# Kernel tuning notes

Measured on AMD Instinct MI355X. Metric: run time of the kernel, lower is better.

Reference implementation:

```python
import jax, jax.numpy as jnp
import numpy as np

N_POINTS = 262144
NUM_ENC = 6      # F
NUM_FEATS = 16   # C
LOG2_RES = 5
STD = 0.2


def setup_inputs() -> dict:
    key = jax.random.key(0)
    k1, k2 = jax.random.split(key)
    points = jax.random.normal(k1, (N_POINTS, 3), dtype=jnp.float32)
    # freqs = 2 ** linspace(0, F-1, F) = [1,2,4,8,16,32]
    freqs = 2.0 ** jnp.linspace(0.0, NUM_ENC - 1.0, NUM_ENC).astype(jnp.float32)
    res = 2 ** LOG2_RES
    features = jax.random.normal(k2, (NUM_ENC * 2 * 3, NUM_FEATS, res, 1), dtype=jnp.float32) * STD
    return {"points": points, "freqs": freqs, "features": features}


def _forward(points, freqs, features):
    n = points.shape[0]
    F = freqs.shape[0]
    C = features.shape[1]
    res = features.shape[2]
    # --- pos_encode ---
    fp = points[:, None, :] * freqs[None, :, None]          # (n, F, 3)
    enc = jnp.stack((jnp.sin(fp), jnp.cos(fp)), axis=-2)    # (n, F, 2, 3)
    encs = enc.reshape(n, F * 2 * 3).T                       # (G=F*2*3, n), values in [-1,1]
    # --- encoder: grid_sample(features, grid=[x=0, y=encs], align_corners=True) ---
    # features: (G, C, H=res, W=1); x=0 with W=1 -> column 0; bilinear only along H.
    g = jnp.transpose(features[..., 0], (0, 2, 1))           # (G, res, C)
    iy = (encs + 1.0) * 0.5 * (res - 1)                      # (G, n), align_corners=True mapping
    iy0 = jnp.floor(iy)
    w1 = iy - iy0                                            # weight for upper neighbor
    i0 = jnp.clip(iy0.astype(jnp.int32), 0, res - 1)
    i1 = jnp.clip(i0 + 1, 0, res - 1)                        # clamp safe: w1==0 at boundary
    take = jax.vmap(lambda tbl, idx: tbl[idx])               # per-grid gather
    v0 = take(g, i0)                                         # (G, n, C)
    v1 = take(g, i1)                                         # (G, n, C)
    fs = v0 * (1.0 - w1)[..., None] + v1 * w1[..., None]     # (G, n, C)
    fs = jnp.swapaxes(fs, 1, 2)                              # (G, C, n), matches torch (G,C,1,N)
    # raw contiguous reinterpretation (36 -> F,3,2) exactly as torch .view does
    fs = fs.reshape(F, 3, 2, C, n) + encs.reshape(F, 3, 2, 1, n)
    return jnp.transpose(fs, (4, 3, 0, 1, 2)).reshape(n, -1)  # (n, C*F*3*2)


def reference(points, freqs, features):
    return _forward(points, freqs, features)
```

## Files before the change

kernel.cpp:

```cpp
#include <hip/hip_runtime.h>

#define NPTS   262144
#define CHUNK  256
#define BLOCK  1024
#define NG     36
#define NC     16
#define RES    32
#define TAB_FLOATS (NG * NC * RES)


__global__ __launch_bounds__(BLOCK) void freqhash_kernel(
    const float* __restrict__ points,
    const float* __restrict__ features,
    float* __restrict__ out)
{
    __shared__ float tab[TAB_FLOATS + 4];
    __shared__ float sval[CHUNK * NG];

    const int t = threadIdx.x;
    const int chunk_base = blockIdx.x * CHUNK;

    {
        const float4* __restrict__ src = (const float4*)features;
        float4* dst = (float4*)tab;
        #pragma unroll
        for (int i = 0; i < TAB_FLOATS / 4 / BLOCK + 1; ++i) {
            int idx = t + i * BLOCK;
            if (idx < TAB_FLOATS / 4) dst[idx] = src[idx];
        }
        if (t == 0) {
            tab[TAB_FLOATS + 0] = 0.f; tab[TAB_FLOATS + 1] = 0.f;
            tab[TAB_FLOATS + 2] = 0.f; tab[TAB_FLOATS + 3] = 0.f;
        }
    }

    {
        const int phat    = t >> 2;
        const int quarter = t & 3;
        const int p = chunk_base + phat;
        const float x = points[p * 3 + 0];
        const float y = points[p * 3 + 1];
        const float z = points[p * 3 + 2];
        #pragma unroll
        for (int k = 0; k < 9; ++k) {
            const int g   = quarter * 9 + k;
            const int f   = g / 6;
            const int rem = g - f * 6;
            const int s   = rem / 3;
            const int d   = rem - s * 3;
            const float coord = (d == 0) ? x : ((d == 1) ? y : z);
            const float freq  = (float)(1 << f);
            const float rev   = coord * freq * 0.15915494309189535f;
            const float r     = __builtin_amdgcn_fractf(rev);
            const float sv    = __builtin_amdgcn_sinf(r);
            const float cv    = __builtin_amdgcn_cosf(r);
            const float val   = s ? cv : sv;
            sval[t * 9 + k] = val;
        }
    }
    __syncthreads();

    float* __restrict__ outp = out + (size_t)chunk_base * (NC * NG);
    #pragma unroll 2
    for (int it = 0; it < (CHUNK * NC * NG / 4) / BLOCK; ++it) {
        const unsigned q    = (unsigned)t + (unsigned)it * BLOCK;
        const unsigned phat = q / 144u;
        const unsigned rq   = q - phat * 144u;
        const unsigned c    = rq / 9u;
        const unsigned g0   = (rq - c * 9u) * 4u;

        const float4 v4 = *(const float4*)&sval[phat * NG + g0];
        const int base = (int)(g0 * NC + c) * RES;

        float res[4];
        const float vv[4] = { v4.x, v4.y, v4.z, v4.w };
        #pragma unroll
        for (int k = 0; k < 4; ++k) {
            const float val = vv[k];
            const float iy  = __builtin_fmaf(val, 15.5f, 15.5f);
            const float fl  = floorf(iy);
            const float w   = iy - fl;
            int i0 = (int)fl;
            i0 = i0 < 0 ? 0 : (i0 > 31 ? 31 : i0);
            const float* __restrict__ row = &tab[base + k * (NC * RES) + i0];
            const float v0 = row[0];
            const float v1 = row[1];
            res[k] = __builtin_fmaf(w, v1 - v0, v0) + val;
        }
        *(float4*)&outp[(size_t)q * 4] = make_float4(res[0], res[1], res[2], res[3]);
    }
}

extern "C" void kernel_launch(void* const* d_in, const int* in_sizes, int n_in,
                              void* d_out, int out_size, void* d_ws, size_t ws_size,
                              hipStream_t stream) {
    const float* points   = (const float*)d_in[0];
    const float* features = (const float*)d_in[2];
    float* out = (float*)d_out;
    freqhash_kernel<<<dim3(NPTS / CHUNK), dim3(BLOCK), 0, stream>>>(points, features, out);
}
```

Measured before the change: 680.3 us.

## Split encode into separate kernel and use persistent grid for table gather

Moves the sin/cos positional encoding into its own kernel that writes the 36 values per point to workspace. The gather kernel becomes a persistent grid of 512 blocks that loads the feature table into shared memory once per block, not once per 256-point chunk, and pads rows to 33 floats to reduce bank conflicts. The cost is an extra launch and a global round trip for the encoded values, and the clamp/floor logic is simplified to a truncating int cast.

```diff
diff --git a/kernel.cpp b/kernel.cpp
--- a/kernel.cpp
+++ b/kernel.cpp
@@ -1,76 +1,69 @@
 #include <hip/hip_runtime.h>
 
 #define NPTS   262144
-#define CHUNK  256
-#define BLOCK  1024
 #define NG     36
 #define NC     16
 #define RES    32
-#define TAB_FLOATS (NG * NC * RES)
+#define NROWS  (NG * NC)
+#define PADR   33
+#define TABF   (NROWS * PADR)
 
+#define K1_BLOCK 256
+#define K2_BLOCK 1024
+#define K2_GRID  512
+#define TOTAL_Q  (NPTS * 144)
+#define K2_ITERS (TOTAL_Q / (K2_BLOCK * K2_GRID))
 
-__global__ __launch_bounds__(BLOCK) void freqhash_kernel(
-    const float* __restrict__ points,
+__global__ __launch_bounds__(K1_BLOCK) void encode_kernel(
+    const float* __restrict__ points, float* __restrict__ sval)
+{
+    const int p = blockIdx.x * K1_BLOCK + threadIdx.x;
+    const float x = points[p * 3 + 0];
+    const float y = points[p * 3 + 1];
+    const float z = points[p * 3 + 2];
+    float v[NG];
+    #pragma unroll
+    for (int f = 0; f < 6; ++f) {
+        const float w = (float)(1 << f) * 0.15915494309189535f;
+        #pragma unroll
+        for (int d = 0; d < 3; ++d) {
+            const float coord = (d == 0) ? x : ((d == 1) ? y : z);
+            const float r = __builtin_amdgcn_fractf(coord * w);
+            v[f * 6 + d]     = __builtin_amdgcn_sinf(r);
+            v[f * 6 + 3 + d] = __builtin_amdgcn_cosf(r);
+        }
+    }
+    float4* __restrict__ dst = (float4*)(sval + (size_t)p * NG);
+    #pragma unroll
+    for (int j = 0; j < 9; ++j) dst[j] = ((const float4*)v)[j];
+}
+
+__global__ __launch_bounds__(K2_BLOCK, 8) void gather_kernel(
     const float* __restrict__ features,
+    const float* __restrict__ sval,
     float* __restrict__ out)
 {
-    __shared__ float tab[TAB_FLOATS + 4];
-    __shared__ float sval[CHUNK * NG];
-
-    const int t = threadIdx.x;
-    const int chunk_base = blockIdx.x * CHUNK;
-
-    {
-        const float4* __restrict__ src = (const float4*)features;
-        float4* dst = (float4*)tab;
-        #pragma unroll
-        for (int i = 0; i < TAB_FLOATS / 4 / BLOCK + 1; ++i) {
-            int idx = t + i * BLOCK;
-            if (idx < TAB_FLOATS / 4) dst[idx] = src[idx];
-        }
-        if (t == 0) {
-            tab[TAB_FLOATS + 0] = 0.f; tab[TAB_FLOATS + 1] = 0.f;
-            tab[TAB_FLOATS + 2] = 0.f; tab[TAB_FLOATS + 3] = 0.f;
-        }
-    }
-
-    {
-        const int phat    = t >> 2;
-        const int quarter = t & 3;
-        const int p = chunk_base + phat;
-        const float x = points[p * 3 + 0];
-        const float y = points[p * 3 + 1];
-        const float z = points[p * 3 + 2];
-        #pragma unroll
-        for (int k = 0; k < 9; ++k) {
-            const int g   = quarter * 9 + k;
-            const int f   = g / 6;
-            const int rem = g - f * 6;
-            const int s   = rem / 3;
-            const int d   = rem - s * 3;
-            const float coord = (d == 0) ? x : ((d == 1) ? y : z);
-            const float freq  = (float)(1 << f);
-            const float rev   = coord * freq * 0.15915494309189535f;
-            const float r     = __builtin_amdgcn_fractf(rev);
-            const float sv    = __builtin_amdgcn_sinf(r);
-            const float cv    = __builtin_amdgcn_cosf(r);
-            const float val   = s ? cv : sv;
-            sval[t * 9 + k] = val;
-        }
+    __shared__ float tab[TABF];
+    for (int idx = threadIdx.x; idx < TABF; idx += K2_BLOCK) {
+        const int row = idx / PADR;
+        const int col = idx - row * PADR;
+        tab[idx] = (col < RES) ? features[row * RES + col] : 0.f;
     }
     __syncthreads();
 
-    float* __restrict__ outp = out + (size_t)chunk_base * (NC * NG);
+    const unsigned tid = blockIdx.x * K2_BLOCK + threadIdx.x;
+    const unsigned T   = K2_BLOCK * K2_GRID;
+    float4* __restrict__ out4 = (float4*)out;
+
     #pragma unroll 2
-    for (int it = 0; it < (CHUNK * NC * NG / 4) / BLOCK; ++it) {
-        const unsigned q    = (unsigned)t + (unsigned)it * BLOCK;
+    for (int it = 0; it < K2_ITERS; ++it) {
+        const unsigned q    = tid + (unsigned)it * T;
         const unsigned phat = q / 144u;
         const unsigned rq   = q - phat * 144u;
         const unsigned c    = rq / 9u;
-        const unsigned g0   = (rq - c * 9u) * 4u;
-
-        const float4 v4 = *(const float4*)&sval[phat * NG + g0];
-        const int base = (int)(g0 * NC + c) * RES;
+        const unsigned m    = rq - c * 9u;
+        const float4 v4 = *(const float4*)&sval[phat * 36u + m * 4u];
+        const int base  = (int)((m * 4u * NC + c) * PADR);
 
         float res[4];
         const float vv[4] = { v4.x, v4.y, v4.z, v4.w };
@@ -78,16 +71,15 @@
         for (int k = 0; k < 4; ++k) {
             const float val = vv[k];
             const float iy  = __builtin_fmaf(val, 15.5f, 15.5f);
-            const float fl  = floorf(iy);
-            const float w   = iy - fl;
-            int i0 = (int)fl;
-            i0 = i0 < 0 ? 0 : (i0 > 31 ? 31 : i0);
-            const float* __restrict__ row = &tab[base + k * (NC * RES) + i0];
+            int i0 = (int)iy;
+            i0 = i0 < 0 ? 0 : (i0 > RES - 1 ? RES - 1 : i0);
+            const float w = iy - (float)i0;
+            const float* __restrict__ row = &tab[base + k * (NC * PADR) + i0];
             const float v0 = row[0];
             const float v1 = row[1];
             res[k] = __builtin_fmaf(w, v1 - v0, v0) + val;
         }
-        *(float4*)&outp[(size_t)q * 4] = make_float4(res[0], res[1], res[2], res[3]);
+        out4[q] = make_float4(res[0], res[1], res[2], res[3]);
     }
 }
 
@@ -96,6 +88,9 @@
                               hipStream_t stream) {
     const float* points   = (const float*)d_in[0];
     const float* features = (const float*)d_in[2];
-    float* out = (float*)d_out;
-    freqhash_kernel<<<dim3(NPTS / CHUNK), dim3(BLOCK), 0, stream>>>(points, features, out);
+    float* out  = (float*)d_out;
+    float* sval = (float*)d_ws;
+
+    encode_kernel<<<dim3(NPTS / K1_BLOCK), dim3(K1_BLOCK), 0, stream>>>(points, sval);
+    gather_kernel<<<dim3(K2_GRID), dim3(K2_BLOCK), 0, stream>>>(features, sval, out);
 }
```

Result: faster. 656.1 us (-3.6%).
